# Performance work log

Measured on AMD Instinct MI355X. Metric: run time of the kernel, lower is better.

## Reference

```python
import jax, jax.numpy as jnp
import numpy as np

# ---- model constants (match init_kwargs) ----
N_USERS = 100_000
N_ITEMS = 50_000
N_ENTITIES = 200_000          # items are entities [0, N_ITEMS)
N_REL = 20                    # relations after the +1 shift; rel_weight has N_REL-1 rows
EMB = 64
HOPS = 2
MARGIN_CCL = 0.8
NUM_NEG = 64
ANGLE_W = 0.1
ANGLE_DROP = 0.5              # eval-mode Dropout(ones)*rate == constant rate scaling
N_EDGES = 1_000_000
NNZ = 1_000_000
N_TRIPLETS = 200_000
BATCH = 4096
EPS = 1e-6


def _l2norm(x):
    # torch F.normalize(dim=-1, eps=1e-12)
    return x / jnp.maximum(jnp.linalg.norm(x, axis=-1, keepdims=True), 1e-12)


def setup_inputs() -> dict:
    key = jax.random.key(0)
    ks = jax.random.split(key, 13)
    # xavier_uniform bounds: sqrt(6/(fan_in+fan_out))
    b_all = float(np.sqrt(6.0 / (N_USERS + N_ENTITIES + EMB)))
    b_cf = float(np.sqrt(6.0 / (N_ITEMS + EMB)))
    b_rel = float(np.sqrt(6.0 / (N_REL - 1 + EMB)))
    all_embed = jax.random.uniform(ks[0], (N_USERS + N_ENTITIES, EMB), jnp.float32, -b_all, b_all)
    item_emb_cf = jax.random.uniform(ks[1], (N_ITEMS, EMB), jnp.float32, -b_cf, b_cf)
    rel_weight = jax.random.uniform(ks[2], (N_REL - 1, EMB), jnp.float32, -b_rel, b_rel)
    # D^{-1/2} A row-normalized positive values
    interact_vals = jax.random.uniform(ks[3], (NNZ,), jnp.float32, 0.01, 0.3)
    user = jax.random.randint(ks[4], (BATCH,), 0, N_USERS)
    pos_item = jax.random.randint(ks[5], (BATCH,), 0, N_ITEMS)
    neg_item = jax.random.randint(ks[6], (BATCH, NUM_NEG), 0, N_ITEMS)
    edge_index = jax.random.randint(ks[7], (2, N_EDGES), 0, N_ENTITIES)
    edge_type = jax.random.randint(ks[8], (N_EDGES,), 1, N_REL)  # relations already +1 shifted
    interact_rows = jax.random.randint(ks[9], (NNZ,), 0, N_USERS)
    interact_cols = jax.random.randint(ks[10], (NNZ,), 0, N_ITEMS)  # URM cols live in item range
    triplet_h = jax.random.randint(ks[11], (N_TRIPLETS,), 0, N_ENTITIES)
    triplet_t = jax.random.randint(ks[12], (N_TRIPLETS,), 0, N_ITEMS)
    return dict(all_embed=all_embed, item_emb_cf=item_emb_cf, rel_weight=rel_weight,
                interact_vals=interact_vals, user=user, pos_item=pos_item, neg_item=neg_item,
                edge_index=edge_index, edge_type=edge_type, interact_rows=interact_rows,
                interact_cols=interact_cols, triplet_h=triplet_h, triplet_t=triplet_t)


def _gcn(user_emb, entity_emb, item_cf, rel_weight, edge_index, edge_type, rows, cols, vals):
    """Multi-hop HAKG GraphConv: relation-gated KG scatter-mean + sparse user/CF aggregation."""
    head, tail = edge_index[0], edge_index[1]
    ent_res, usr_res, cf_res = entity_emb, user_emb, item_cf
    cnt = jax.ops.segment_sum(jnp.ones(head.shape, entity_emb.dtype), head, N_ENTITIES)
    denom = jnp.maximum(cnt, 1.0)[:, None]            # scatter_mean denominator
    rel_e = rel_weight[edge_type - 1]                 # [E, D]
    for _ in range(HOPS):
        # KG aggregate: entity_agg[h] = mean_{(h,r,t)} entity[t] * rel[r]
        neigh = entity_emb[tail] * rel_e              # [E, D]
        entity_agg = jax.ops.segment_sum(neigh, head, N_ENTITIES) / denom
        # user aggregate: sparse interact_mat @ entity_emb
        user_agg = jax.ops.segment_sum(vals[:, None] * entity_emb[cols], rows, N_USERS)
        # CF branch (LightGCN-style): R @ item_cf then R^T @ (...)
        u_cf = jax.ops.segment_sum(vals[:, None] * item_cf[cols], rows, N_USERS)
        item_agg_cf = jax.ops.segment_sum(vals[:, None] * u_cf[rows], cols, N_ITEMS)
        entity_emb = _l2norm(entity_agg)
        user_emb = _l2norm(user_agg)
        item_cf = _l2norm(item_agg_cf)
        ent_res = ent_res + entity_emb
        usr_res = usr_res + user_emb
        cf_res = cf_res + item_cf
    return ent_res, usr_res, cf_res


def _half_aperture(u):
    K = 0.1
    sqnu = jnp.clip(jnp.sum(u * u, -1), 0.0, 1.0 - EPS)
    return jnp.arcsin(jnp.clip(K * (1.0 - sqnu) / jnp.sqrt(sqnu), -1.0 + EPS, 1.0 - EPS))


def _angle_at_u(u, v):
    nu = jnp.linalg.norm(u, axis=-1)
    nv = jnp.linalg.norm(v, axis=-1)
    dp = jnp.sum(u * v, -1)
    ed = jnp.linalg.norm(u - v, axis=-1)
    num = dp * (1.0 + nu ** 2) - nu ** 2 * (1.0 + nv ** 2)
    den = nu * ed * jnp.sqrt(jnp.clip(1.0 + nv ** 2 * nu ** 2 - 2.0 * dp, EPS, None)) + EPS
    return jnp.arccos(jnp.clip(num / den, -1.0 + EPS, 1.0 - EPS))


def _contrastive_loss(u_e, pos_e, neg_e, pos_cf, neg_cf):
    B = u_e.shape[0]
    u, p, n = _l2norm(u_e), _l2norm(pos_e), _l2norm(neg_e)
    pcf, ncf = _l2norm(pos_cf), _l2norm(neg_cf)
    ui_pos = jax.nn.relu(2.0 - (jnp.sum(u * p, -1) + jnp.sum(u * pcf, -1)))
    ub = jnp.repeat(u, NUM_NEG, axis=0)               # [B*K, D]
    def neg_loss(nn_):
        s = jax.nn.relu(jnp.sum(ub * nn_, -1) - MARGIN_CCL).reshape(B, NUM_NEG)
        return jnp.sum(s, -1) / (jnp.sum(s > 0, -1).astype(s.dtype) + 1e-5)
    return jnp.mean(ui_pos + neg_loss(n) + neg_loss(ncf))


def reference(all_embed, item_emb_cf, rel_weight, interact_vals, user, pos_item, neg_item,
              edge_index, edge_type, interact_rows, interact_cols, triplet_h, triplet_t):
    user_emb = all_embed[:N_USERS]
    entity_emb = all_embed[N_USERS:]
    ent_g, usr_g, cf_g = _gcn(user_emb, entity_emb, item_emb_cf, rel_weight,
                              edge_index, edge_type, interact_rows, interact_cols, interact_vals)
    flat_neg = neg_item.reshape(-1)
    u_e = usr_g[user]
    loss1 = _contrastive_loss(u_e, ent_g[pos_item], ent_g[flat_neg], cf_g[pos_item], cf_g[flat_neg])
    # angle (hierarchy) loss, vectorized over all cross-type triplets
    hs = entity_emb[triplet_h] * ANGLE_DROP
    ts = entity_emb[triplet_t] * ANGLE_DROP
    angle_half = jax.nn.relu(_angle_at_u(hs, ts) - _half_aperture(hs))
    loss2 = ANGLE_W * jnp.sum(angle_half) / N_TRIPLETS
    return loss1 + loss2
```

## Files before the change

kernel.cpp:

```cpp
#include <hip/hip_runtime.h>
#include <math.h>

#define N_USERS    100000
#define N_ITEMS    50000
#define N_ENTITIES 200000
#define N_REL      20
#define EMB        64
#define HOPS       2
#define MARGIN_CCL 0.8f
#define NUM_NEG    64
#define ANGLE_W    0.1f
#define ANGLE_DROP 0.5f
#define N_EDGES    1000000
#define NNZ        1000000
#define N_TRIPLETS 200000
#define BATCH      4096
#define EPSF       1e-6f

#define TILE1 4096
#define NBUCK 196
#define BCAP  9216
#define ACAP  8192
#define HBLK  ((N_EDGES + TILE1 - 1) / TILE1)
#define P1B   (3 * HBLK)
#define KGB   (N_ENTITIES / 32)
#define UCFB  (N_USERS / 32)
#define ITEMB ((N_ITEMS + 31) / 32)
#define UBB   (BATCH / 32)
#define ANGB  (N_TRIPLETS / 32)
#define LOSSB (BATCH / 4)
#define CONVE (N_ENTITIES * 16 / 256)
#define CONVI (N_ITEMS * 16 / 256)

typedef _Float16 half4_t __attribute__((ext_vector_type(4)));
typedef _Float16 half8_t __attribute__((ext_vector_type(8)));
typedef float float8_t __attribute__((ext_vector_type(8)));

__device__ inline float4 h2f(half4_t h) {
    return make_float4((float)h.x, (float)h.y, (float)h.z, (float)h.w);
}
__device__ inline half4_t f2h(float4 f) {
    half4_t h; h.x = (_Float16)f.x; h.y = (_Float16)f.y;
    h.z = (_Float16)f.z; h.w = (_Float16)f.w; return h;
}
__device__ inline float8_t h8_to_f8(half8_t h) { return __builtin_convertvector(h, float8_t); }
__device__ inline half8_t f8_to_h8(float8_t f) { return __builtin_convertvector(f, half8_t); }
__device__ inline half8_t h8_zero() {
    half8_t z;
    #pragma unroll
    for (int i = 0; i < 8; ++i) z[i] = (_Float16)0.0f;
    return z;
}
__device__ inline float sum_sq8(float8_t f) {
    float s = 0.f;
    #pragma unroll
    for (int i = 0; i < 8; ++i) s += f[i] * f[i];
    return s;
}
__device__ inline float dot8(float8_t a, float8_t b) {
    float s = 0.f;
    #pragma unroll
    for (int i = 0; i < 8; ++i) s += a[i] * b[i];
    return s;
}
__device__ inline float8_t f8_from2(float4 lo, float4 hi) {
    float8_t f;
    f[0] = lo.x; f[1] = lo.y; f[2] = lo.z; f[3] = lo.w;
    f[4] = hi.x; f[5] = hi.y; f[6] = hi.z; f[7] = hi.w;
    return f;
}
__device__ inline float grp_red8(float v) {
    v += __shfl_xor(v, 1, 64); v += __shfl_xor(v, 2, 64); v += __shfl_xor(v, 4, 64);
    return v;
}
__device__ inline float dot4(float4 a, float4 b) {
    return a.x * b.x + a.y * b.y + a.z * b.z + a.w * b.w;
}
__device__ inline float grp_red16(float v) {
    v += __shfl_xor(v, 1, 64); v += __shfl_xor(v, 2, 64);
    v += __shfl_xor(v, 4, 64); v += __shfl_xor(v, 8, 64);
    return v;
}
__device__ inline float cross_grp_scalar(float v) {
    v += __shfl_xor(v, 16, 64); v += __shfl_xor(v, 32, 64);
    return v;
}

__global__ void __launch_bounds__(256) prep_kernel(
        const float4* __restrict__ ent0, const float4* __restrict__ cf0,
        half4_t* __restrict__ ent_a, half4_t* __restrict__ cf16_a,
        int* __restrict__ bcur_e, int* __restrict__ bcur_u, int* __restrict__ bcur_i) {
    int bx = blockIdx.x, t = threadIdx.x;
    if (bx < CONVE) { int i = bx * 256 + t; ent_a[i] = f2h(ent0[i]); return; }
    bx -= CONVE;
    if (bx < CONVI) { int i = bx * 256 + t; cf16_a[i] = f2h(cf0[i]); return; }
    if (t < NBUCK) {
        bcur_e[t] = t * ACAP;
        bcur_u[t] = t * ACAP;
        bcur_i[t] = t * ACAP;
    }
}

__device__ inline void angle_body(int ablk, int t, const half8_t* __restrict__ ent_h,
                                  const int* __restrict__ th, const int* __restrict__ tt,
                                  float* sb, float* __restrict__ l2blk) {
    int o = t & 7;
    int grp = t >> 3;
    int trip = ablk * 32 + grp;
    int h = th[trip], t2 = tt[trip];
    float8_t hv = h8_to_f8(ent_h[h * 8 + o]);
    float8_t tv = h8_to_f8(ent_h[t2 * 8 + o]);
    hv *= ANGLE_DROP;
    tv *= ANGLE_DROP;
    float8_t dv = hv - tv;
    float s_hh = grp_red8(sum_sq8(hv));
    float s_tt = grp_red8(sum_sq8(tv));
    float s_ht = grp_red8(dot8(hv, tv));
    float s_dd = grp_red8(sum_sq8(dv));
    if (o == 0) {
        float nu = sqrtf(s_hh);
        float ed = sqrtf(s_dd);
        float sqnu = fminf(fmaxf(s_hh, 0.0f), 1.0f - EPSF);
        float ha_arg = fminf(fmaxf(0.1f * (1.0f - sqnu) / sqrtf(sqnu), -1.0f + EPSF), 1.0f - EPSF);
        float half_ap = asinf(ha_arg);
        float num = s_ht * (1.0f + s_hh) - s_hh * (1.0f + s_tt);
        float den = nu * ed * sqrtf(fmaxf(1.0f + s_tt * s_hh - 2.0f * s_ht, EPSF)) + EPSF;
        float ang = acosf(fminf(fmaxf(num / den, -1.0f + EPSF), 1.0f - EPSF));
        sb[grp] = fmaxf(ang - half_ap, 0.0f);
    }
    __syncthreads();
    if (t == 0) {
        float tot = 0.f;
        #pragma unroll
        for (int i = 0; i < 32; ++i) tot += sb[i];
        l2blk[ablk] = tot;
    }
}

__global__ void __launch_bounds__(256) phase1_angle(
        const int* __restrict__ head, const int* __restrict__ tail,
        const int* __restrict__ etype, const int* __restrict__ rows,
        const int* __restrict__ cols, const float* __restrict__ vals,
        int* __restrict__ bcur_e, int* __restrict__ bcur_u, int* __restrict__ bcur_i,
        int* __restrict__ keys_e, int* __restrict__ kg_pay,
        int2* __restrict__ u_pay, int2* __restrict__ i_pay,
        const half8_t* __restrict__ ent_a, const int* __restrict__ th,
        const int* __restrict__ tt, float* __restrict__ l2blk) {
    __shared__ int2 pay_st[TILE1];
    __shared__ int lhist[256], lstart[256], lcur[256], gbase[256];
    __shared__ float sb[32];
    int bx = blockIdx.x, t = threadIdx.x;
    if (bx >= P1B) {
        angle_body(bx - P1B, t, ent_a, th, tt, sb, l2blk);
        return;
    }
    int seg = bx / HBLK;
    int tb  = bx % HBLK;
    int tstart = tb * TILE1;
    int valid = min(TILE1, N_EDGES - tstart);
    const int* karr = (seg == 0) ? head : (seg == 1) ? rows : cols;
    int shift = (seg == 0) ? 10 : (seg == 1) ? 9 : 8;
    int* bcur = (seg == 0) ? bcur_e : (seg == 1) ? bcur_u : bcur_i;
    lhist[t] = 0;
    __syncthreads();
    for (int i = t; i < valid; i += 256) atomicAdd(&lhist[karr[tstart + i] >> shift], 1);
    __syncthreads();
    int v = lhist[t];
    lstart[t] = v;
    __syncthreads();
    for (int d = 1; d < 256; d <<= 1) {
        int x = (t >= d) ? lstart[t - d] : 0;
        __syncthreads();
        lstart[t] += x;
        __syncthreads();
    }
    int excl = lstart[t] - v;
    lstart[t] = excl;
    lcur[t] = excl;
    gbase[t] = atomicAdd(&bcur[t], v);
    __syncthreads();
    if (seg == 0) {
        int* key_st = (int*)pay_st;
        int* ps = key_st + TILE1;
        for (int i = t; i < valid; i += 256) {
            int h = head[tstart + i];
            int p = tail[tstart + i] | ((etype[tstart + i] - 1) << 18);
            int sp = atomicAdd(&lcur[h >> 10], 1);
            key_st[sp] = h;
            ps[sp] = p;
        }
        __syncthreads();
        for (int j = t; j < valid; j += 256) {
            int k = key_st[j];
            int b = k >> 10;
            int pos = gbase[b] + (j - lstart[b]);
            keys_e[pos] = k;
            kg_pay[pos] = ps[j];
        }
    } else {
        int2* pay = (seg == 1) ? u_pay : i_pay;
        for (int i = t; i < valid; i += 256) {
            int k = karr[tstart + i];
            int px;
            if (seg == 1) px = cols[tstart + i] | ((k & 511) << 16);
            else          px = rows[tstart + i] | ((k & 255) << 17);
            int2 p = make_int2(px, __float_as_int(vals[tstart + i]));
            int sp = atomicAdd(&lcur[k >> shift], 1);
            pay_st[sp] = p;
        }
        __syncthreads();
        for (int j = t; j < valid; j += 256) {
            int2 p = pay_st[j];
            int lo = 0, hi = 255;
            while (lo < hi) {
                int mid = (lo + hi + 1) >> 1;
                if (lstart[mid] <= j) lo = mid; else hi = mid - 1;
            }
            int bb = lo;
            int pos = gbase[bb] + (j - lstart[bb]);
            pay[pos] = p;
        }
    }
}

__global__ void __launch_bounds__(256) phase2_all(
        const int* __restrict__ bcur_e, const int* __restrict__ keys_e,
        int* __restrict__ kg_pay, int* __restrict__ off_e,
        const int* __restrict__ bcur_u, int2* __restrict__ u_pay, int* __restrict__ off_u,
        const int* __restrict__ bcur_i, int2* __restrict__ i_pay, int* __restrict__ off_i) {
    __shared__ int hist[1024];
    __shared__ int s[256];
    __shared__ int2 lout2[BCAP];
    int seg = blockIdx.x / NBUCK;
    int b   = blockIdx.x % NBUCK;
    int t = threadIdx.x;
    int bins  = (seg == 0) ? 1024 : (seg == 1) ? 512 : 256;
    int shift = (seg == 0) ? 10 : (seg == 1) ? 9 : 8;
    int n_rows = (seg == 0) ? N_ENTITIES : (seg == 1) ? N_USERS : N_ITEMS;
    const int* bcur = (seg == 0) ? bcur_e : (seg == 1) ? bcur_u : bcur_i;
    int* off = (seg == 0) ? off_e : (seg == 1) ? off_u : off_i;
    int rs = b << shift;
    int re = min(rs + bins, n_rows);
    int nr = re - rs;
    int base = b * ACAP;
    int len = bcur[b] - base;
    for (int r = t; r < bins; r += 256) hist[r] = 0;
    __syncthreads();
    if (seg == 0) {
        for (int j = t; j < len; j += 256) atomicAdd(&hist[keys_e[base + j] - rs], 1);
    } else if (seg == 1) {
        for (int j = t; j < len; j += 256) atomicAdd(&hist[(u_pay[base + j].x >> 16) & 511], 1);
    } else {
        for (int j = t; j < len; j += 256) atomicAdd(&hist[(i_pay[base + j].x >> 17) & 255], 1);
    }
    __syncthreads();
    int own = bins >> 8;
    int c[4]; int tot = 0;
    #pragma unroll 4
    for (int i = 0; i < own; ++i) { c[i] = hist[t * own + i]; tot += c[i]; }
    s[t] = tot;
    __syncthreads();
    for (int d = 1; d < 256; d <<= 1) {
        int x = (t >= d) ? s[t - d] : 0;
        __syncthreads();
        s[t] += x;
        __syncthreads();
    }
    int run = s[t] - tot;
    #pragma unroll 4
    for (int i = 0; i < own; ++i) { hist[t * own + i] = run; run += c[i]; }
    __syncthreads();
    for (int r = t; r < nr; r += 256) off[rs + b + r] = base + hist[r];
    if (t == 0) off[rs + b + nr] = base + len;
    __syncthreads();
    if (seg == 0) {
        int* lo = (int*)lout2;
        for (int j = t; j < len; j += 256) {
            int k = keys_e[base + j];
            int slot = atomicAdd(&hist[k - rs], 1);
            lo[slot] = kg_pay[base + j];
        }
        __syncthreads();
        for (int j = t; j < len; j += 256) kg_pay[base + j] = lo[j];
    } else {
        int2* pay = (seg == 1) ? u_pay : i_pay;
        int sh = (seg == 1) ? 16 : 17;
        int msk = (seg == 1) ? 511 : 255;
        for (int j = t; j < len; j += 256) {
            int2 p = pay[base + j];
            int slot = atomicAdd(&hist[(p.x >> sh) & msk], 1);
            lout2[slot] = p;
        }
        __syncthreads();
        for (int j = t; j < len; j += 256) pay[base + j] = lout2[j];
    }
}

__device__ inline void kg0_body(int bid, int t, const int* __restrict__ off,
                                const int* __restrict__ pack, half8_t* srel,
                                const float* __restrict__ relw,
                                const half8_t* __restrict__ src, half8_t* __restrict__ dst,
                                half8_t* __restrict__ res, const float4* __restrict__ res_init) {
    if (t < (N_REL - 1) * 8) {
        int rel = t >> 3, o = t & 7;
        const float4* r4 = (const float4*)relw;
        srel[rel * 9 + o] = f8_to_h8(f8_from2(r4[rel * 16 + o * 2], r4[rel * 16 + o * 2 + 1]));
    }
    __syncthreads();
    int row = bid * 32 + (t >> 3);
    int o = t & 7;
    int idx = row + (row >> 10);
    int s = off[idx], e = off[idx + 1];
    half8_t acc = h8_zero();
    int k = s;
    for (; k + 2 <= e; k += 2) {
        int p0 = pack[k], p1 = pack[k + 1];
        half8_t a0 = src[(p0 & 0x3FFFF) * 8 + o];
        half8_t b0 = srel[(p0 >> 18) * 9 + o];
        half8_t a1 = src[(p1 & 0x3FFFF) * 8 + o];
        half8_t b1 = srel[(p1 >> 18) * 9 + o];
        acc += a0 * b0;
        acc += a1 * b1;
    }
    if (k < e) {
        int p0 = pack[k];
        acc += src[(p0 & 0x3FFFF) * 8 + o] * srel[(p0 >> 18) * 9 + o];
    }
    float8_t f = h8_to_f8(acc);
    f *= 1.0f / fmaxf((float)(e - s), 1.0f);
    float ss = grp_red8(sum_sq8(f));
    f *= 1.0f / fmaxf(sqrtf(ss), 1e-12f);
    dst[row * 8 + o] = f8_to_h8(f);
    if (row < N_ITEMS) {
        float8_t rr = f8_from2(res_init[row * 16 + o * 2], res_init[row * 16 + o * 2 + 1]);
        rr += f;
        res[row * 8 + o] = f8_to_h8(rr);
    }
}

__device__ inline void kg2_body(int bid, int t, const int* __restrict__ off,
                                const int* __restrict__ pack, half8_t* srel,
                                const float* __restrict__ relw,
                                const half8_t* __restrict__ src, half8_t* __restrict__ res) {
    if (t < (N_REL - 1) * 8) {
        int rel = t >> 3, o = t & 7;
        const float4* r4 = (const float4*)relw;
        srel[rel * 9 + o] = f8_to_h8(f8_from2(r4[rel * 16 + o * 2], r4[rel * 16 + o * 2 + 1]));
    }
    __syncthreads();
    int row = bid * 32 + (t >> 3);
    if (row >= N_ITEMS) return;
    int o = t & 7;
    int idx = row + (row >> 10);
    int s = off[idx], e = off[idx + 1];
    half8_t acc = h8_zero();
    int k = s;
    for (; k + 2 <= e; k += 2) {
        int p0 = pack[k], p1 = pack[k + 1];
        half8_t a0 = src[(p0 & 0x3FFFF) * 8 + o];
        half8_t b0 = srel[(p0 >> 18) * 9 + o];
        half8_t a1 = src[(p1 & 0x3FFFF) * 8 + o];
        half8_t b1 = srel[(p1 >> 18) * 9 + o];
        acc += a0 * b0;
        acc += a1 * b1;
    }
    if (k < e) {
        int p0 = pack[k];
        acc += src[(p0 & 0x3FFFF) * 8 + o] * srel[(p0 >> 18) * 9 + o];
    }
    float8_t f = h8_to_f8(acc);
    f *= 1.0f / fmaxf((float)(e - s), 1.0f);
    float ss = grp_red8(sum_sq8(f));
    f *= 1.0f / fmaxf(sqrtf(ss), 1e-12f);
    float8_t rr = h8_to_f8(res[row * 8 + o]);
    rr += f;
    float s2 = grp_red8(sum_sq8(rr));
    rr *= 1.0f / fmaxf(sqrtf(s2), 1e-12f);
    res[row * 8 + o] = f8_to_h8(rr);
}

__device__ inline void ucf_body(int bid, int t, const int* __restrict__ off,
                                const int2* __restrict__ u_pack,
                                const half8_t* __restrict__ cf16,
                                half8_t* __restrict__ ucf) {
    int row = bid * 32 + (t >> 3);
    int o = t & 7;
    int idx = row + (row >> 9);
    int s = off[idx], e = off[idx + 1];
    half8_t acc = h8_zero();
    int k = s;
    for (; k + 2 <= e; k += 2) {
        int2 p0 = u_pack[k], p1 = u_pack[k + 1];
        _Float16 v0 = (_Float16)__int_as_float(p0.y);
        _Float16 v1 = (_Float16)__int_as_float(p1.y);
        acc += cf16[(p0.x & 0xFFFF) * 8 + o] * v0;
        acc += cf16[(p1.x & 0xFFFF) * 8 + o] * v1;
    }
    if (k < e) {
        int2 p0 = u_pack[k];
        acc += cf16[(p0.x & 0xFFFF) * 8 + o] * (_Float16)__int_as_float(p0.y);
    }
    ucf[row * 8 + o] = acc;
}

__device__ inline void ubatch_body(int bid, int t, const int* __restrict__ user,
                                   const int* __restrict__ off,
                                   const int2* __restrict__ u_pack,
                                   const half8_t* __restrict__ ent_a,
                                   const half8_t* __restrict__ ent_b,
                                   const float4* __restrict__ usr0f,
                                   half8_t* __restrict__ usr_b) {
    int g = t >> 3, o = t & 7;
    int b = bid * 32 + g;
    int uid = user[b];
    int idx = uid + (uid >> 9);
    int s = off[idx], e = off[idx + 1];
    half8_t acc1 = h8_zero(), acc2 = h8_zero();
    int k = s;
    for (; k + 2 <= e; k += 2) {
        int2 p0 = u_pack[k], p1 = u_pack[k + 1];
        int c0 = (p0.x & 0xFFFF) * 8 + o;
        int c1 = (p1.x & 0xFFFF) * 8 + o;
        _Float16 v0 = (_Float16)__int_as_float(p0.y);
        _Float16 v1 = (_Float16)__int_as_float(p1.y);
        acc1 += ent_a[c0] * v0;
        acc2 += ent_b[c0] * v0;
        acc1 += ent_a[c1] * v1;
        acc2 += ent_b[c1] * v1;
    }
    if (k < e) {
        int2 p0 = u_pack[k];
        int c0 = (p0.x & 0xFFFF) * 8 + o;
        _Float16 v0 = (_Float16)__int_as_float(p0.y);
        acc1 += ent_a[c0] * v0;
        acc2 += ent_b[c0] * v0;
    }
    float8_t f1 = h8_to_f8(acc1);
    float ss1 = grp_red8(sum_sq8(f1));
    f1 *= 1.0f / fmaxf(sqrtf(ss1), 1e-12f);
    float8_t u0 = f8_from2(usr0f[uid * 16 + o * 2], usr0f[uid * 16 + o * 2 + 1]);
    float8_t r1 = h8_to_f8(f8_to_h8(u0 + f1));
    float8_t f2 = h8_to_f8(acc2);
    float ss2 = grp_red8(sum_sq8(f2));
    f2 *= 1.0f / fmaxf(sqrtf(ss2), 1e-12f);
    float8_t r = r1 + f2;
    float s3 = grp_red8(sum_sq8(r));
    r *= 1.0f / fmaxf(sqrtf(s3), 1e-12f);
    usr_b[b * 8 + o] = f8_to_h8(r);
}

__device__ inline void item_body(int bid, int t, const int* __restrict__ off,
                                 const int2* __restrict__ i_pack,
                                 const half8_t* __restrict__ ucf,
                                 half8_t* __restrict__ cf_nxt, half8_t* __restrict__ res,
                                 const float4* __restrict__ res_init, int first, int last) {
    int row = bid * 32 + (t >> 3);
    int o = t & 7;
    if (row >= N_ITEMS) return;
    int idx = row + (row >> 8);
    int s = off[idx], e = off[idx + 1];
    half8_t acc = h8_zero();
    int k = s;
    for (; k + 2 <= e; k += 2) {
        int2 p0 = i_pack[k], p1 = i_pack[k + 1];
        _Float16 v0 = (_Float16)__int_as_float(p0.y);
        _Float16 v1 = (_Float16)__int_as_float(p1.y);
        acc += ucf[(p0.x & 0x1FFFF) * 8 + o] * v0;
        acc += ucf[(p1.x & 0x1FFFF) * 8 + o] * v1;
    }
    if (k < e) {
        int2 p0 = i_pack[k];
        acc += ucf[(p0.x & 0x1FFFF) * 8 + o] * (_Float16)__int_as_float(p0.y);
    }
    float8_t f = h8_to_f8(acc);
    float ss = grp_red8(sum_sq8(f));
    f *= 1.0f / fmaxf(sqrtf(ss), 1e-12f);
    if (!last) cf_nxt[row * 8 + o] = f8_to_h8(f);
    float8_t rr;
    if (first) rr = f8_from2(res_init[row * 16 + o * 2], res_init[row * 16 + o * 2 + 1]);
    else       rr = h8_to_f8(res[row * 8 + o]);
    rr += f;
    if (last) {
        float s2 = grp_red8(sum_sq8(rr));
        rr *= 1.0f / fmaxf(sqrtf(s2), 1e-12f);
    }
    res[row * 8 + o] = f8_to_h8(rr);
}

__device__ inline void loss_ent_body(int b, int t,
                                     const int* __restrict__ pos, const int* __restrict__ neg,
                                     const half4_t* __restrict__ usrb4,
                                     const half4_t* __restrict__ ent4,
                                     float* __restrict__ dpe, float* __restrict__ l1pe) {
    int lane = t & 63;
    int g = lane >> 4, q = lane & 15;
    int pid = pos[b];
    float4 u = h2f(usrb4[b * 16 + q]);
    float4 p = h2f(ent4[pid * 16 + q]);
    float dpe_v = grp_red16(dot4(u, p));
    float sum_n = 0.f, cnt_n = 0.f;
    const int* nb = neg + b * NUM_NEG;
    for (int j = 0; j < NUM_NEG; j += 8) {
        int n0 = nb[j + g], n1 = nb[j + 4 + g];
        float dn0 = grp_red16(dot4(u, h2f(ent4[n0 * 16 + q])));
        float dn1 = grp_red16(dot4(u, h2f(ent4[n1 * 16 + q])));
        float s0 = fmaxf(dn0 - MARGIN_CCL, 0.f); sum_n += s0; if (s0 > 0.f) cnt_n += 1.f;
        float s1 = fmaxf(dn1 - MARGIN_CCL, 0.f); sum_n += s1; if (s1 > 0.f) cnt_n += 1.f;
    }
    sum_n = cross_grp_scalar(sum_n); cnt_n = cross_grp_scalar(cnt_n);
    if (lane == 0) {
        dpe[b] = dpe_v;
        l1pe[b] = sum_n / (cnt_n + 1e-5f);
    }
}

__global__ void __launch_bounds__(256) loss_cf_kernel(
        const int* __restrict__ pos, const int* __restrict__ neg,
        const half4_t* __restrict__ usrb4, const half4_t* __restrict__ cf4,
        const float* __restrict__ dpe, const float* __restrict__ l1pe,
        float* __restrict__ l1p) {
    int b = blockIdx.x * 4 + (threadIdx.x >> 6);
    int lane = threadIdx.x & 63;
    int g = lane >> 4, q = lane & 15;
    int pid = pos[b];
    float4 u = h2f(usrb4[b * 16 + q]);
    float4 pc = h2f(cf4[pid * 16 + q]);
    float dpc = grp_red16(dot4(u, pc));
    float sum_c = 0.f, cnt_c = 0.f;
    const int* nb = neg + b * NUM_NEG;
    for (int j = 0; j < NUM_NEG; j += 8) {
        int n0 = nb[j + g], n1 = nb[j + 4 + g];
        float dc0 = grp_red16(dot4(u, h2f(cf4[n0 * 16 + q])));
        float dc1 = grp_red16(dot4(u, h2f(cf4[n1 * 16 + q])));
        float t0 = fmaxf(dc0 - MARGIN_CCL, 0.f); sum_c += t0; if (t0 > 0.f) cnt_c += 1.f;
        float t1 = fmaxf(dc1 - MARGIN_CCL, 0.f); sum_c += t1; if (t1 > 0.f) cnt_c += 1.f;
    }
    sum_c = cross_grp_scalar(sum_c); cnt_c = cross_grp_scalar(cnt_c);
    if (lane == 0) {
        float ui_pos = fmaxf(2.0f - dpe[b] - dpc, 0.0f);
        l1p[b] = ui_pos + l1pe[b] + sum_c / (cnt_c + 1e-5f);
    }
}

__global__ void __launch_bounds__(256) fused_h0(
        const int* __restrict__ off_e, const int* __restrict__ kg_pack,
        const float* __restrict__ relw, const half8_t* __restrict__ ent_a,
        half8_t* __restrict__ ent_b, half8_t* __restrict__ ent_res,
        const float4* __restrict__ ent0f,
        const int* __restrict__ off_u, const int2* __restrict__ u_pack,
        const half8_t* __restrict__ cf16_a, half8_t* __restrict__ ucf) {
    __shared__ half8_t srel[(N_REL - 1) * 9];
    int bx = blockIdx.x, t = threadIdx.x;
    if (bx < KGB) {
        kg0_body(bx, t, off_e, kg_pack, srel, relw, ent_a, ent_b, ent_res, ent0f);
    } else {
        ucf_body(bx - KGB, t, off_u, u_pack, cf16_a, ucf);
    }
}

__global__ void __launch_bounds__(256) fused_ik(
        const int* __restrict__ off_e, const int* __restrict__ kg_pack,
        const float* __restrict__ relw, const half8_t* __restrict__ ent_b,
        half8_t* __restrict__ ent_res,
        const int* __restrict__ off_i, const int2* __restrict__ i_pack,
        const half8_t* __restrict__ ucf, half8_t* __restrict__ cf16_b,
        half8_t* __restrict__ cf_res, const float4* __restrict__ cf0f,
        const int* __restrict__ user, const int* __restrict__ off_u,
        const int2* __restrict__ u_pack, const half8_t* __restrict__ ent_a,
        const float4* __restrict__ usr0f, half8_t* __restrict__ usr_b) {
    __shared__ half8_t srel[(N_REL - 1) * 9];
    int bx = blockIdx.x, t = threadIdx.x;
    if (bx < ITEMB) {
        kg2_body(bx, t, off_e, kg_pack, srel, relw, ent_b, ent_res);
    } else if (bx < 2 * ITEMB) {
        item_body(bx - ITEMB, t, off_i, i_pack, ucf, cf16_b, cf_res, cf0f, 1, 0);
    } else {
        ubatch_body(bx - 2 * ITEMB, t, user, off_u, u_pack, ent_a, ent_b, usr0f, usr_b);
    }
}

__global__ void __launch_bounds__(256) fused_u1_loss(
        const int* __restrict__ off_u, const int2* __restrict__ u_pack,
        const half8_t* __restrict__ cf16_b, half8_t* __restrict__ ucf,
        const int* __restrict__ pos, const int* __restrict__ neg,
        const half4_t* __restrict__ usrb4, const half4_t* __restrict__ ent4,
        float* __restrict__ dpe, float* __restrict__ l1pe) {
    int bx = blockIdx.x, t = threadIdx.x;
    if (bx < UCFB) {
        ucf_body(bx, t, off_u, u_pack, cf16_b, ucf);
    } else {
        int b = (bx - UCFB) * 4 + (t >> 6);
        loss_ent_body(b, t, pos, neg, usrb4, ent4, dpe, l1pe);
    }
}

__global__ void __launch_bounds__(256) item_h1(
        const int* __restrict__ off_i, const int2* __restrict__ i_pack,
        const half8_t* __restrict__ ucf, half8_t* __restrict__ cf_res,
        const float4* __restrict__ cf0f) {
    item_body(blockIdx.x, threadIdx.x, off_i, i_pack, ucf, (half8_t*)0, cf_res, cf0f, 0, 1);
}

__global__ void finalize_kernel(const float* __restrict__ l1p, const float* __restrict__ l2b,
                                float* __restrict__ out) {
    __shared__ float sb[1024];
    float a1 = 0.f;
    for (int i = threadIdx.x; i < BATCH; i += 1024) a1 += l1p[i];
    float a2 = 0.f;
    for (int i = threadIdx.x; i < ANGB; i += 1024) a2 += l2b[i];
    sb[threadIdx.x] = a1 / (float)BATCH + ANGLE_W * a2 / (float)N_TRIPLETS;
    __syncthreads();
    for (int s = 512; s > 0; s >>= 1) {
        if (threadIdx.x < s) sb[threadIdx.x] += sb[threadIdx.x + s];
        __syncthreads();
    }
    if (threadIdx.x == 0) out[0] = sb[0];
}

extern "C" void kernel_launch(void* const* d_in, const int* in_sizes, int n_in,
                              void* d_out, int out_size, void* d_ws, size_t ws_size,
                              hipStream_t stream) {
    const float* all_embed = (const float*)d_in[0];
    const float* item_cf0  = (const float*)d_in[1];
    const float* relw      = (const float*)d_in[2];
    const float* vals      = (const float*)d_in[3];
    const int* user        = (const int*)d_in[4];
    const int* pos_item    = (const int*)d_in[5];
    const int* neg_item    = (const int*)d_in[6];
    const int* edge_head   = (const int*)d_in[7];
    const int* edge_tail   = edge_head + N_EDGES;
    const int* etype       = (const int*)d_in[8];
    const int* irows       = (const int*)d_in[9];
    const int* icols       = (const int*)d_in[10];
    const int* th          = (const int*)d_in[11];
    const int* tt          = (const int*)d_in[12];
    float* out             = (float*)d_out;

    char* base = (char*)d_ws;
    size_t woff = 0;
    auto alloc = [&](size_t bytes) -> void* {
        void* p = base + woff;
        woff = (woff + bytes + 255) & ~(size_t)255;
        return p;
    };
    half8_t* ent_a   = (half8_t*)alloc((size_t)N_ENTITIES * EMB * 2);
    half8_t* ent_b   = (half8_t*)alloc((size_t)N_ENTITIES * EMB * 2);
    half8_t* cf16_a  = (half8_t*)alloc((size_t)N_ITEMS * EMB * 2);
    half8_t* cf16_b  = (half8_t*)alloc((size_t)N_ITEMS * EMB * 2);
    half8_t* ucf     = (half8_t*)alloc((size_t)N_USERS * EMB * 2);
    half8_t* ent_res = (half8_t*)alloc((size_t)N_ITEMS * EMB * 2);
    half8_t* cf_res  = (half8_t*)alloc((size_t)N_ITEMS * EMB * 2);
    half8_t* usr_b   = (half8_t*)alloc((size_t)BATCH * EMB * 2);
    int2* u_pack     = (int2*)alloc((size_t)NBUCK * ACAP * 8);
    int2* i_pack     = (int2*)alloc((size_t)NBUCK * ACAP * 8);
    int* kg_pack     = (int*)alloc((size_t)NBUCK * ACAP * 4);
    int* keys_e      = (int*)alloc((size_t)NBUCK * ACAP * 4);
    float* l1p       = (float*)alloc((size_t)BATCH * 4);
    float* dpe       = (float*)alloc((size_t)BATCH * 4);
    float* l1pe      = (float*)alloc((size_t)BATCH * 4);
    float* l2blk     = (float*)alloc((size_t)ANGB * 4);
    int* off_e       = (int*)alloc((size_t)(N_ENTITIES + NBUCK + 1) * 4);
    int* off_u       = (int*)alloc((size_t)(N_USERS + NBUCK + 1) * 4);
    int* off_i       = (int*)alloc((size_t)(N_ITEMS + NBUCK + 1) * 4);
    int* bcur_e      = (int*)alloc(256 * 4);
    int* bcur_u      = (int*)alloc(256 * 4);
    int* bcur_i      = (int*)alloc(256 * 4);

    const float* ent0 = all_embed + (size_t)N_USERS * EMB;

    prep_kernel<<<CONVE + CONVI + 1, 256, 0, stream>>>(
        (const float4*)ent0, (const float4*)item_cf0, (half4_t*)ent_a, (half4_t*)cf16_a,
        bcur_e, bcur_u, bcur_i);
    phase1_angle<<<P1B + ANGB, 256, 0, stream>>>(
        edge_head, edge_tail, etype, irows, icols, vals,
        bcur_e, bcur_u, bcur_i, keys_e, kg_pack, u_pack, i_pack,
        ent_a, th, tt, l2blk);
    phase2_all<<<3 * NBUCK, 256, 0, stream>>>(bcur_e, keys_e, kg_pack, off_e,
                                              bcur_u, u_pack, off_u,
                                              bcur_i, i_pack, off_i);
    fused_h0<<<KGB + UCFB, 256, 0, stream>>>(
        off_e, kg_pack, relw, ent_a, ent_b, ent_res, (const float4*)ent0,
        off_u, u_pack, cf16_a, ucf);
    fused_ik<<<2 * ITEMB + UBB, 256, 0, stream>>>(
        off_e, kg_pack, relw, ent_b, ent_res,
        off_i, i_pack, ucf, cf16_b, cf_res, (const float4*)item_cf0,
        user, off_u, u_pack, ent_a, (const float4*)all_embed, usr_b);
    fused_u1_loss<<<UCFB + LOSSB, 256, 0, stream>>>(
        off_u, u_pack, cf16_b, ucf, pos_item, neg_item,
        (const half4_t*)usr_b, (const half4_t*)ent_res, dpe, l1pe);
    item_h1<<<ITEMB, 256, 0, stream>>>(off_i, i_pack, ucf, cf_res,
                                       (const float4*)item_cf0);
    loss_cf_kernel<<<LOSSB, 256, 0, stream>>>(pos_item, neg_item,
                                              (const half4_t*)usr_b, (const half4_t*)cf_res,
                                              dpe, l1pe, l1p);
    finalize_kernel<<<1, 1024, 0, stream>>>(l1p, l2blk, out);
}
```

Measured before the change: 356.5 us.

## Restructure sort pipeline: ping buffers, wave scans, fp16 payload, relocate conversions and angle

Phase 2 now writes the bucketed payloads directly from ping buffers (aliased onto later-used embedding buffers) into final packed arrays, replacing the large LDS staging tile and copy-back. Block-level prefix scans switch from shared-memory Hillis-Steele loops to wave shuffle scans. The interaction value is stored as fp16 bits alongside the bucket id, so phase 1 drops its per-element binary search. The fp32→fp16 conversion moves into the phase-1 launch and the angle loss moves into fused_h0, aiming to shrink LDS use, raise occupancy and improve overlap, at the cost of fragile buffer aliasing.

Result: no change. 357.9 us (+0.4%).

```diff
diff --git a/kernel.cpp b/kernel.cpp
--- a/kernel.cpp
+++ b/kernel.cpp
@@ -19,7 +19,6 @@
 
 #define TILE1 4096
 #define NBUCK 196
-#define BCAP  9216
 #define ACAP  8192
 #define HBLK  ((N_EDGES + TILE1 - 1) / TILE1)
 #define P1B   (3 * HBLK)
@@ -85,15 +84,17 @@
     v += __shfl_xor(v, 16, 64); v += __shfl_xor(v, 32, 64);
     return v;
 }
+__device__ inline int f32_to_h16bits(float v) {
+    _Float16 h = (_Float16)v;
+    return (int)__builtin_bit_cast(unsigned short, h);
+}
+__device__ inline _Float16 h16_from_bits(int b) {
+    return __builtin_bit_cast(_Float16, (unsigned short)(b & 0xFFFF));
+}
 
 __global__ void __launch_bounds__(256) prep_kernel(
-        const float4* __restrict__ ent0, const float4* __restrict__ cf0,
-        half4_t* __restrict__ ent_a, half4_t* __restrict__ cf16_a,
         int* __restrict__ bcur_e, int* __restrict__ bcur_u, int* __restrict__ bcur_i) {
-    int bx = blockIdx.x, t = threadIdx.x;
-    if (bx < CONVE) { int i = bx * 256 + t; ent_a[i] = f2h(ent0[i]); return; }
-    bx -= CONVE;
-    if (bx < CONVI) { int i = bx * 256 + t; cf16_a[i] = f2h(cf0[i]); return; }
+    int t = threadIdx.x;
     if (t < NBUCK) {
         bcur_e[t] = t * ACAP;
         bcur_u[t] = t * ACAP;
@@ -137,21 +138,23 @@
     }
 }
 
-__global__ void __launch_bounds__(256) phase1_angle(
+__global__ void __launch_bounds__(256) phase1_sort(
         const int* __restrict__ head, const int* __restrict__ tail,
         const int* __restrict__ etype, const int* __restrict__ rows,
         const int* __restrict__ cols, const float* __restrict__ vals,
         int* __restrict__ bcur_e, int* __restrict__ bcur_u, int* __restrict__ bcur_i,
-        int* __restrict__ keys_e, int* __restrict__ kg_pay,
-        int2* __restrict__ u_pay, int2* __restrict__ i_pay,
-        const half8_t* __restrict__ ent_a, const int* __restrict__ th,
-        const int* __restrict__ tt, float* __restrict__ l2blk) {
+        int* __restrict__ keys_ping, int* __restrict__ kg_ping,
+        int2* __restrict__ u_ping, int2* __restrict__ i_ping,
+        const float4* __restrict__ ent0, const float4* __restrict__ cf0,
+        half4_t* __restrict__ ent_a4, half4_t* __restrict__ cf16a4) {
     __shared__ int2 pay_st[TILE1];
     __shared__ int lhist[256], lstart[256], lcur[256], gbase[256];
-    __shared__ float sb[32];
+    __shared__ int wsum[4], wpre[4];
     int bx = blockIdx.x, t = threadIdx.x;
     if (bx >= P1B) {
-        angle_body(bx - P1B, t, ent_a, th, tt, sb, l2blk);
+        int cb = bx - P1B;
+        if (cb < CONVE) { int i = cb * 256 + t; ent_a4[i] = f2h(ent0[i]); }
+        else            { int i = (cb - CONVE) * 256 + t; cf16a4[i] = f2h(cf0[i]); }
         return;
     }
     int seg = bx / HBLK;
@@ -166,15 +169,22 @@
     for (int i = t; i < valid; i += 256) atomicAdd(&lhist[karr[tstart + i] >> shift], 1);
     __syncthreads();
     int v = lhist[t];
-    lstart[t] = v;
-    __syncthreads();
-    for (int d = 1; d < 256; d <<= 1) {
-        int x = (t >= d) ? lstart[t - d] : 0;
-        __syncthreads();
-        lstart[t] += x;
-        __syncthreads();
-    }
-    int excl = lstart[t] - v;
+    int lane = t & 63, wv = t >> 6;
+    int sc = v;
+    #pragma unroll
+    for (int d = 1; d < 64; d <<= 1) {
+        int x = __shfl_up(sc, d, 64);
+        if (lane >= d) sc += x;
+    }
+    if (lane == 63) wsum[wv] = sc;
+    __syncthreads();
+    if (t == 0) {
+        int a = 0;
+        #pragma unroll
+        for (int i = 0; i < 4; ++i) { wpre[i] = a; a += wsum[i]; }
+    }
+    __syncthreads();
+    int excl = sc + wpre[wv] - v;
     lstart[t] = excl;
     lcur[t] = excl;
     gbase[t] = atomicAdd(&bcur[t], v);
@@ -194,29 +204,25 @@
             int k = key_st[j];
             int b = k >> 10;
             int pos = gbase[b] + (j - lstart[b]);
-            keys_e[pos] = k;
-            kg_pay[pos] = ps[j];
+            keys_ping[pos] = k;
+            kg_ping[pos] = ps[j];
         }
     } else {
-        int2* pay = (seg == 1) ? u_pay : i_pay;
+        int2* pay = (seg == 1) ? u_ping : i_ping;
         for (int i = t; i < valid; i += 256) {
             int k = karr[tstart + i];
+            int bkt = k >> shift;
             int px;
             if (seg == 1) px = cols[tstart + i] | ((k & 511) << 16);
             else          px = rows[tstart + i] | ((k & 255) << 17);
-            int2 p = make_int2(px, __float_as_int(vals[tstart + i]));
-            int sp = atomicAdd(&lcur[k >> shift], 1);
-            pay_st[sp] = p;
+            int py = f32_to_h16bits(vals[tstart + i]) | (bkt << 16);
+            int sp = atomicAdd(&lcur[bkt], 1);
+            pay_st[sp] = make_int2(px, py);
         }
         __syncthreads();
         for (int j = t; j < valid; j += 256) {
             int2 p = pay_st[j];
-            int lo = 0, hi = 255;
-            while (lo < hi) {
-                int mid = (lo + hi + 1) >> 1;
-                if (lstart[mid] <= j) lo = mid; else hi = mid - 1;
-            }
-            int bb = lo;
+            int bb = (p.y >> 16) & 0xFF;
             int pos = gbase[bb] + (j - lstart[bb]);
             pay[pos] = p;
         }
@@ -224,13 +230,14 @@
 }
 
 __global__ void __launch_bounds__(256) phase2_all(
-        const int* __restrict__ bcur_e, const int* __restrict__ keys_e,
-        int* __restrict__ kg_pay, int* __restrict__ off_e,
-        const int* __restrict__ bcur_u, int2* __restrict__ u_pay, int* __restrict__ off_u,
-        const int* __restrict__ bcur_i, int2* __restrict__ i_pay, int* __restrict__ off_i) {
+        const int* __restrict__ bcur_e, const int* __restrict__ keys_ping,
+        const int* __restrict__ kg_ping, int* __restrict__ kg_pack, int* __restrict__ off_e,
+        const int* __restrict__ bcur_u, const int2* __restrict__ u_ping,
+        int2* __restrict__ u_pack, int* __restrict__ off_u,
+        const int* __restrict__ bcur_i, const int2* __restrict__ i_ping,
+        int2* __restrict__ i_pack, int* __restrict__ off_i) {
     __shared__ int hist[1024];
-    __shared__ int s[256];
-    __shared__ int2 lout2[BCAP];
+    __shared__ int wsum[4], wpre[4];
     int seg = blockIdx.x / NBUCK;
     int b   = blockIdx.x % NBUCK;
     int t = threadIdx.x;
@@ -247,52 +254,57 @@
     for (int r = t; r < bins; r += 256) hist[r] = 0;
     __syncthreads();
     if (seg == 0) {
-        for (int j = t; j < len; j += 256) atomicAdd(&hist[keys_e[base + j] - rs], 1);
+        for (int j = t; j < len; j += 256) atomicAdd(&hist[keys_ping[base + j] - rs], 1);
     } else if (seg == 1) {
-        for (int j = t; j < len; j += 256) atomicAdd(&hist[(u_pay[base + j].x >> 16) & 511], 1);
+        for (int j = t; j < len; j += 256) atomicAdd(&hist[(u_ping[base + j].x >> 16) & 511], 1);
     } else {
-        for (int j = t; j < len; j += 256) atomicAdd(&hist[(i_pay[base + j].x >> 17) & 255], 1);
+        for (int j = t; j < len; j += 256) atomicAdd(&hist[(i_ping[base + j].x >> 17) & 255], 1);
     }
     __syncthreads();
     int own = bins >> 8;
     int c[4]; int tot = 0;
-    #pragma unroll 4
-    for (int i = 0; i < own; ++i) { c[i] = hist[t * own + i]; tot += c[i]; }
-    s[t] = tot;
-    __syncthreads();
-    for (int d = 1; d < 256; d <<= 1) {
-        int x = (t >= d) ? s[t - d] : 0;
-        __syncthreads();
-        s[t] += x;
-        __syncthreads();
-    }
-    int run = s[t] - tot;
-    #pragma unroll 4
-    for (int i = 0; i < own; ++i) { hist[t * own + i] = run; run += c[i]; }
+    #pragma unroll
+    for (int i = 0; i < 4; ++i) { c[i] = (i < own) ? hist[t * own + i] : 0; tot += c[i]; }
+    int lane = t & 63, wv = t >> 6;
+    int sc = tot;
+    #pragma unroll
+    for (int d = 1; d < 64; d <<= 1) {
+        int x = __shfl_up(sc, d, 64);
+        if (lane >= d) sc += x;
+    }
+    if (lane == 63) wsum[wv] = sc;
+    __syncthreads();
+    if (t == 0) {
+        int a = 0;
+        #pragma unroll
+        for (int i = 0; i < 4; ++i) { wpre[i] = a; a += wsum[i]; }
+    }
+    __syncthreads();
+    int run = sc + wpre[wv] - tot;
+    #pragma unroll
+    for (int i = 0; i < 4; ++i) { if (i < own) { hist[t * own + i] = run; run += c[i]; } }
     __syncthreads();
     for (int r = t; r < nr; r += 256) off[rs + b + r] = base + hist[r];
     if (t == 0) off[rs + b + nr] = base + len;
     __syncthreads();
     if (seg == 0) {
-        int* lo = (int*)lout2;
         for (int j = t; j < len; j += 256) {
-            int k = keys_e[base + j];
+            int k = keys_ping[base + j];
             int slot = atomicAdd(&hist[k - rs], 1);
-            lo[slot] = kg_pay[base + j];
+            kg_pack[base + slot] = kg_ping[base + j];
         }
-        __syncthreads();
-        for (int j = t; j < len; j += 256) kg_pay[base + j] = lo[j];
+    } else if (seg == 1) {
+        for (int j = t; j < len; j += 256) {
+            int2 p = u_ping[base + j];
+            int slot = atomicAdd(&hist[(p.x >> 16) & 511], 1);
+            u_pack[base + slot] = p;
+        }
     } else {
-        int2* pay = (seg == 1) ? u_pay : i_pay;
-        int sh = (seg == 1) ? 16 : 17;
-        int msk = (seg == 1) ? 511 : 255;
         for (int j = t; j < len; j += 256) {
-            int2 p = pay[base + j];
-            int slot = atomicAdd(&hist[(p.x >> sh) & msk], 1);
-            lout2[slot] = p;
+            int2 p = i_ping[base + j];
+            int slot = atomicAdd(&hist[(p.x >> 17) & 255], 1);
+            i_pack[base + slot] = p;
         }
-        __syncthreads();
-        for (int j = t; j < len; j += 256) pay[base + j] = lout2[j];
     }
 }
 
@@ -391,14 +403,14 @@
     int k = s;
     for (; k + 2 <= e; k += 2) {
         int2 p0 = u_pack[k], p1 = u_pack[k + 1];
-        _Float16 v0 = (_Float16)__int_as_float(p0.y);
-        _Float16 v1 = (_Float16)__int_as_float(p1.y);
+        _Float16 v0 = h16_from_bits(p0.y);
+        _Float16 v1 = h16_from_bits(p1.y);
         acc += cf16[(p0.x & 0xFFFF) * 8 + o] * v0;
         acc += cf16[(p1.x & 0xFFFF) * 8 + o] * v1;
     }
     if (k < e) {
         int2 p0 = u_pack[k];
-        acc += cf16[(p0.x & 0xFFFF) * 8 + o] * (_Float16)__int_as_float(p0.y);
+        acc += cf16[(p0.x & 0xFFFF) * 8 + o] * h16_from_bits(p0.y);
     }
     ucf[row * 8 + o] = acc;
 }
@@ -421,8 +433,8 @@
         int2 p0 = u_pack[k], p1 = u_pack[k + 1];
         int c0 = (p0.x & 0xFFFF) * 8 + o;
         int c1 = (p1.x & 0xFFFF) * 8 + o;
-        _Float16 v0 = (_Float16)__int_as_float(p0.y);
-        _Float16 v1 = (_Float16)__int_as_float(p1.y);
+        _Float16 v0 = h16_from_bits(p0.y);
+        _Float16 v1 = h16_from_bits(p1.y);
         acc1 += ent_a[c0] * v0;
         acc2 += ent_b[c0] * v0;
         acc1 += ent_a[c1] * v1;
@@ -431,7 +443,7 @@
     if (k < e) {
         int2 p0 = u_pack[k];
         int c0 = (p0.x & 0xFFFF) * 8 + o;
-        _Float16 v0 = (_Float16)__int_as_float(p0.y);
+        _Float16 v0 = h16_from_bits(p0.y);
         acc1 += ent_a[c0] * v0;
         acc2 += ent_b[c0] * v0;
     }
@@ -463,14 +475,14 @@
     int k = s;
     for (; k + 2 <= e; k += 2) {
         int2 p0 = i_pack[k], p1 = i_pack[k + 1];
-        _Float16 v0 = (_Float16)__int_as_float(p0.y);
-        _Float16 v1 = (_Float16)__int_as_float(p1.y);
+        _Float16 v0 = h16_from_bits(p0.y);
+        _Float16 v1 = h16_from_bits(p1.y);
         acc += ucf[(p0.x & 0x1FFFF) * 8 + o] * v0;
         acc += ucf[(p1.x & 0x1FFFF) * 8 + o] * v1;
     }
     if (k < e) {
         int2 p0 = i_pack[k];
-        acc += ucf[(p0.x & 0x1FFFF) * 8 + o] * (_Float16)__int_as_float(p0.y);
+        acc += ucf[(p0.x & 0x1FFFF) * 8 + o] * h16_from_bits(p0.y);
     }
     float8_t f = h8_to_f8(acc);
     float ss = grp_red8(sum_sq8(f));
@@ -548,13 +560,18 @@
         half8_t* __restrict__ ent_b, half8_t* __restrict__ ent_res,
         const float4* __restrict__ ent0f,
         const int* __restrict__ off_u, const int2* __restrict__ u_pack,
-        const half8_t* __restrict__ cf16_a, half8_t* __restrict__ ucf) {
+        const half8_t* __restrict__ cf16_a, half8_t* __restrict__ ucf,
+        const int* __restrict__ th, const int* __restrict__ tt,
+        float* __restrict__ l2blk) {
     __shared__ half8_t srel[(N_REL - 1) * 9];
+    __shared__ float sb[32];
     int bx = blockIdx.x, t = threadIdx.x;
     if (bx < KGB) {
         kg0_body(bx, t, off_e, kg_pack, srel, relw, ent_a, ent_b, ent_res, ent0f);
+    } else if (bx < KGB + UCFB) {
+        ucf_body(bx - KGB, t, off_u, u_pack, cf16_a, ucf);
     } else {
-        ucf_body(bx - KGB, t, off_u, u_pack, cf16_a, ucf);
+        angle_body(bx - KGB - UCFB, t, ent_a, th, tt, sb, l2blk);
     }
 }
 
@@ -643,18 +660,20 @@
         woff = (woff + bytes + 255) & ~(size_t)255;
         return p;
     };
+    const size_t ping_ui = (size_t)NBUCK * ACAP * 8;
+    const size_t ping_kg = (size_t)NBUCK * ACAP * 4;
+
     half8_t* ent_a   = (half8_t*)alloc((size_t)N_ENTITIES * EMB * 2);
-    half8_t* ent_b   = (half8_t*)alloc((size_t)N_ENTITIES * EMB * 2);
+    half8_t* ent_b   = (half8_t*)alloc(2 * ping_ui);
     half8_t* cf16_a  = (half8_t*)alloc((size_t)N_ITEMS * EMB * 2);
-    half8_t* cf16_b  = (half8_t*)alloc((size_t)N_ITEMS * EMB * 2);
+    half8_t* cf16_b  = (half8_t*)alloc(ping_kg);
     half8_t* ucf     = (half8_t*)alloc((size_t)N_USERS * EMB * 2);
     half8_t* ent_res = (half8_t*)alloc((size_t)N_ITEMS * EMB * 2);
     half8_t* cf_res  = (half8_t*)alloc((size_t)N_ITEMS * EMB * 2);
     half8_t* usr_b   = (half8_t*)alloc((size_t)BATCH * EMB * 2);
-    int2* u_pack     = (int2*)alloc((size_t)NBUCK * ACAP * 8);
-    int2* i_pack     = (int2*)alloc((size_t)NBUCK * ACAP * 8);
-    int* kg_pack     = (int*)alloc((size_t)NBUCK * ACAP * 4);
-    int* keys_e      = (int*)alloc((size_t)NBUCK * ACAP * 4);
+    int2* u_pack     = (int2*)alloc(ping_ui);
+    int2* i_pack     = (int2*)alloc(ping_ui);
+    int* kg_pack     = (int*)alloc(ping_kg);
     float* l1p       = (float*)alloc((size_t)BATCH * 4);
     float* dpe       = (float*)alloc((size_t)BATCH * 4);
     float* l1pe      = (float*)alloc((size_t)BATCH * 4);
@@ -666,21 +685,24 @@
     int* bcur_u      = (int*)alloc(256 * 4);
     int* bcur_i      = (int*)alloc(256 * 4);
 
+    int2* u_ping   = (int2*)ent_b;
+    int2* i_ping   = (int2*)((char*)ent_b + ping_ui);
+    int* kg_ping   = (int*)cf16_b;
+    int* keys_ping = (int*)ucf;
+
     const float* ent0 = all_embed + (size_t)N_USERS * EMB;
 
-    prep_kernel<<<CONVE + CONVI + 1, 256, 0, stream>>>(
-        (const float4*)ent0, (const float4*)item_cf0, (half4_t*)ent_a, (half4_t*)cf16_a,
-        bcur_e, bcur_u, bcur_i);
-    phase1_angle<<<P1B + ANGB, 256, 0, stream>>>(
+    prep_kernel<<<1, 256, 0, stream>>>(bcur_e, bcur_u, bcur_i);
+    phase1_sort<<<P1B + CONVE + CONVI, 256, 0, stream>>>(
         edge_head, edge_tail, etype, irows, icols, vals,
-        bcur_e, bcur_u, bcur_i, keys_e, kg_pack, u_pack, i_pack,
-        ent_a, th, tt, l2blk);
-    phase2_all<<<3 * NBUCK, 256, 0, stream>>>(bcur_e, keys_e, kg_pack, off_e,
-                                              bcur_u, u_pack, off_u,
-                                              bcur_i, i_pack, off_i);
-    fused_h0<<<KGB + UCFB, 256, 0, stream>>>(
+        bcur_e, bcur_u, bcur_i, keys_ping, kg_ping, u_ping, i_ping,
+        (const float4*)ent0, (const float4*)item_cf0, (half4_t*)ent_a, (half4_t*)cf16_a);
+    phase2_all<<<3 * NBUCK, 256, 0, stream>>>(bcur_e, keys_ping, kg_ping, kg_pack, off_e,
+                                              bcur_u, u_ping, u_pack, off_u,
+                                              bcur_i, i_ping, i_pack, off_i);
+    fused_h0<<<KGB + UCFB + ANGB, 256, 0, stream>>>(
         off_e, kg_pack, relw, ent_a, ent_b, ent_res, (const float4*)ent0,
-        off_u, u_pack, cf16_a, ucf);
+        off_u, u_pack, cf16_a, ucf, th, tt, l2blk);
     fused_ik<<<2 * ITEMB + UBB, 256, 0, stream>>>(
         off_e, kg_pack, relw, ent_b, ent_res,
         off_i, i_pack, ucf, cf16_b, cf_res, (const float4*)item_cf0,
```
